# Kernel optimization log

Measured on AMD Instinct MI355X. Metric: run time of the kernel, lower is better.

## Reference

```python
import jax, jax.numpy as jnp
import numpy as np
from math import factorial, sqrt, pi

L = 10  # must match init_kwargs


def setup_inputs() -> dict:
    key = jax.random.key(0)
    pos = jax.random.normal(key, (2_000_000, 3), dtype=jnp.float32)
    return {"pos": pos}


def _cpow_tables(zr, zi, nmax):
    """Powers (zr + i*zi)^n for n=0..nmax. Returns (nmax+1, N) real and imag parts.
    Matches powcmplx in the source (repeated complex multiply), computed once."""
    reals = [jnp.ones_like(zr)]
    imags = [jnp.zeros_like(zr)]
    for _ in range(nmax):
        r, im = reals[-1], imags[-1]
        reals.append(zr * r - zi * im)
        imags.append(zr * im + zi * r)
    return jnp.stack(reals), jnp.stack(imags)


def reference(pos):
    norms = jnp.linalg.norm(pos, axis=1)            # (N,)
    mask = (norms > 0).astype(pos.dtype)            # replaces boolean indexing ids
    x, y, x0 = pos[:, 0], pos[:, 1], pos[:, 2]
    xpl1r, xpl1i = -0.5 * x, -0.5 * y
    xm1r, xm1i = 0.5 * x, -0.5 * y
    # precompute all needed complex powers (same math as powcmplx, deduplicated)
    z1r_t, z1i_t = _cpow_tables(xpl1r, xpl1i, L)    # (L+1, N)
    z2r_t, z2i_t = _cpow_tables(xm1r, xm1i, L)

    clms = [None] * ((L + 1) ** 2)
    i = 0
    for l in range(L + 1):
        rl = norms ** l
        for M in range(-l, 1):
            m = abs(M)
            shr = jnp.zeros_like(x)
            shi = jnp.zeros_like(x)
            for p in range(l + 1):
                q = p - m
                s = l - p - q
                if q >= 0 and s >= 0:
                    z1r, z1i = z1r_t[p], z1i_t[p]
                    z2r, z2i = z2r_t[q], z2i_t[q]
                    # NOTE: faithful to source, including its quirks:
                    # zreal uses z1r**2 - z2i**2, and the term is scaled by x0
                    # (x0**s is computed in the source but never used).
                    zreal = z1r ** 2 - z2i ** 2
                    zimag = z1r * z2i + z1i * z2r
                    c = 1.0 / (factorial(p) * factorial(q) * factorial(s))
                    shr = shr + zreal * x0 * c
                    shi = shi + zimag * x0 * c
            scale = sqrt(factorial(l + m) * factorial(l - m)) * sqrt((2 * l + 1) / (4.0 * pi))
            clm_r = jnp.sum(shr * rl * mask) * scale
            clm_i = jnp.sum(shi * rl * mask) * scale
            if m == 0:
                clms[i] = clm_r
            else:
                f = sqrt(2.0) * (-1) ** m
                clms[i] = f * clm_i
                clms[i + 2 * m] = f * clm_r
            i += 1
        i += l
    return jnp.stack(clms).reshape(-1, 1)  # ((L+1)^2, 1)
```

## Files before the change

kernel.cpp:

```cpp
#include <hip/hip_runtime.h>

namespace {

constexpr int LMAX = 10;
constexpr double PI_D = 3.14159265358979323846;

constexpr double dfact(int n) {
    double r = 1.0;
    for (int i = 2; i <= n; ++i) r *= (double)i;
    return r;
}

constexpr double csqrt(double x) {
    if (x <= 0.0) return 0.0;
    double g = x > 1.0 ? x : 1.0;
    for (int i = 0; i < 100; ++i) g = 0.5 * (g + x / g);
    return g;
}

constexpr double FACT[LMAX + 1] = {1., 1., 2., 6., 24., 120., 720., 5040., 40320., 362880., 3628800.};

constexpr int slot_r(int l, int m) { return l * l + m; }
constexpr int slot_i(int l, int m) { return l * l + (l + 1) + (m - 1); }
constexpr int NA = (LMAX + 1) * (LMAX + 1);

constexpr float ci_coef(int l, int m, int q) {
    const double c = 1.0 / (FACT[q + m] * FACT[q] * FACT[l - m - 2 * q]);
    return (q & 1) ? (float)(-c) : (float)c;
}

struct Tables {
    int   map[NA];
    float scl[NA];
};

constexpr Tables make_tables() {
    Tables t{};
    for (int l = 0; l <= LMAX; ++l) {
        for (int m = 0; m <= l; ++m) {
            const int k = slot_r(l, m);
            const double scale =
                csqrt(dfact(l + m) * dfact(l - m)) * csqrt((2 * l + 1) / (4.0 * PI_D));
            const double fold = (m >= 1 && (l - m) <= 1) ? 1.0 / (dfact(m) * dfact(l - m)) : 1.0;
            if (m == 0) {
                t.map[k] = l * l + l;
                t.scl[k] = (float)(scale * fold);
            } else {
                const double f = csqrt(2.0) * ((m & 1) ? -1.0 : 1.0);
                t.map[k] = l * l + l + m;
                t.scl[k] = (float)(f * scale * fold);
            }
        }
        for (int m = 1; m <= l; ++m) {
            const int k = slot_i(l, m);
            const double scale =
                csqrt(dfact(l + m) * dfact(l - m)) * csqrt((2 * l + 1) / (4.0 * PI_D));
            const double f    = csqrt(2.0) * ((m & 1) ? -1.0 : 1.0);
            const double fold = ((l - m) <= 1) ? 1.0 / (dfact(m) * dfact(l - m)) : 1.0;
            t.map[k] = l * l + l - m;
            t.scl[k] = (float)(f * scale * fold);
        }
    }
    return t;
}

__constant__ Tables c_tab = make_tables();

}

__global__ __launch_bounds__(256, 2) void sht_kernel(const float* __restrict__ pos,
                                                     float* __restrict__ out, int n, int nblk) {
    constexpr int PL = LMAX;
    constexpr int QX = PL / 2;

    float acc[NA];
#pragma unroll
    for (int k = 0; k < NA; ++k) acc[k] = 0.f;

    const int tid    = (int)blockIdx.x * 256 + (int)threadIdx.x;
    const int stride = nblk * 256;

    int   i = tid;
    float x = 0.f, y = 0.f, z0 = 0.f;
    if (i < n) {
        x  = pos[3 * i + 0];
        y  = pos[3 * i + 1];
        z0 = pos[3 * i + 2];
    }

    while (i < n) {
        const int inext = i + stride;
        float     px = 0.f, py = 0.f, pz = 0.f;
        if (inext < n) {
            px = pos[3 * inext + 0];
            py = pos[3 * inext + 1];
            pz = pos[3 * inext + 2];
        }

        const float r2  = x * x + y * y + z0 * z0;
        const float nrm = sqrtf(r2);
        const float w0  = (nrm > 0.f) ? z0 : 0.f;

        const float ar  = -0.5f * x, ai = -0.5f * y;
        const float rho = ar * ar + ai * ai;

        float zi[PL + 1], sr[PL + 1], si[QX + 1];
        zi[0] = 0.f;
        sr[0] = 1.f;
        si[0] = 0.f;
        float zrc = 1.f;
#pragma unroll
        for (int p = 1; p <= PL; ++p) {
            const float nzr = ar * zrc - ai * zi[p - 1];
            zi[p]           = ar * zi[p - 1] + ai * zrc;
            zrc             = nzr;
            sr[p]           = zrc * zrc;
            if (p <= QX) si[p] = zi[p] * zi[p];
        }
        float rp[PL + 1];
        rp[0] = 1.f;
#pragma unroll
        for (int l = 1; l <= PL; ++l) rp[l] = rp[l - 1] * nrm;

#pragma unroll
        for (int l = 0; l <= LMAX; ++l) {
            const float wrl = w0 * rp[l];
#pragma unroll
            for (int m = 0; m <= l; ++m) {
                const int Q = (l - m) >> 1;
                if (m >= 1 && Q == 0) {
                    acc[slot_r(l, m)] += sr[m] * wrl;
                    acc[slot_i(l, m)] += zi[m] * wrl;
                } else {
                    float shr = 0.f;
#pragma unroll
                    for (int p = m; 2 * p <= l + m; ++p) {
                        const int   q  = p - m;
                        const float cr = (float)(1.0 / (FACT[p] * FACT[q] * FACT[l - 2 * p + m]));
                        shr += (sr[p] - si[q]) * cr;
                    }
                    acc[slot_r(l, m)] += shr * wrl;
                    if (m >= 1) {
                        float t = ci_coef(l, m, Q);
#pragma unroll
                        for (int q = Q - 1; q >= 0; --q) t = t * rho + ci_coef(l, m, q);
                        acc[slot_i(l, m)] += (t * zi[m]) * wrl;
                    }
                }
            }
        }

        i  = inext;
        x  = px;
        y  = py;
        z0 = pz;
    }

    __shared__ float red[4][NA];
    const int lane = threadIdx.x & 63;
    const int wav  = threadIdx.x >> 6;
#pragma unroll
    for (int k = 0; k < NA; ++k) {
        float v = acc[k];
#pragma unroll
        for (int off = 32; off > 0; off >>= 1) v += __shfl_down(v, off, 64);
        if (lane == 0) red[wav][k] = v;
    }
    __syncthreads();
    if ((int)threadIdx.x < NA) {
        const int   k = (int)threadIdx.x;
        const float v = red[0][k] + red[1][k] + red[2][k] + red[3][k];
        atomicAdd(&out[c_tab.map[k]], v * c_tab.scl[k]);
    }
}

extern "C" void kernel_launch(void* const* d_in, const int* in_sizes, int n_in,
                              void* d_out, int out_size, void* d_ws, size_t ws_size,
                              hipStream_t stream) {
    const float* pos = (const float*)d_in[0];
    float* out       = (float*)d_out;
    const int n      = in_sizes[0] / 3;

    hipMemsetAsync(d_out, 0, (size_t)out_size * sizeof(float), stream);

    const int threads = 256;
    const int blocks = 512;
    sht_kernel<<<blocks, threads, 0, stream>>>(pos, out, n, blocks);
}
```

Before: 126.7 us.

## Accumulate per-power moments and combine linearly in a separate kernel

The real-part sums are linear in the per-point powers sr[p] and si[q] times r^l, so the kernel now accumulates those raw moments per point and applies the factorial coefficients afterwards in a small combine kernel. This removes the inner coefficient sums from the hot loop. Work is also split by l parity across block pairs, which lowers the accumulators per thread and register pressure, but each point is loaded and its powers computed twice. The change adds a workspace memset, a second kernel launch and a different float summation order.

New measurement: 119.4 us. -5.8%, faster.

```diff
diff --git a/kernel.cpp b/kernel.cpp
--- a/kernel.cpp
+++ b/kernel.cpp
@@ -20,64 +20,129 @@
 
 constexpr double FACT[LMAX + 1] = {1., 1., 2., 6., 24., 120., 720., 5040., 40320., 362880., 3628800.};
 
-constexpr int slot_r(int l, int m) { return l * l + m; }
-constexpr int slot_i(int l, int m) { return l * l + (l + 1) + (m - 1); }
-constexpr int NA = (LMAX + 1) * (LMAX + 1);
+constexpr int NM_M = 66;
+constexpr int mi(int p, int l) { return l * (l + 1) / 2 + p; }
+constexpr int ni_base(int l) {
+    int c = 0;
+    for (int ll = 0; ll < l; ++ll) c += ll / 2;
+    return c;
+}
+constexpr int ni(int q, int l) { return NM_M + ni_base(l) + (q - 1); }
+constexpr int NM_N  = 25;
+constexpr int NMOM  = NM_M + NM_N;
+constexpr int ZSLOT = NMOM;
+constexpr int WS_FLOATS = NMOM + 1;
+
+constexpr int part_lmax(int part) { return part ? 9 : 10; }
+constexpr int nls(int part) { return part ? 5 : 6; }
+constexpr int lidx(int part, int l) { return (l - part) >> 1; }
+constexpr int nM(int part) { int c = 0; for (int l = part; l <= LMAX; l += 2) c += l + 1; return c; }
+constexpr int nN(int part) { int c = 0; for (int l = part; l <= LMAX; l += 2) c += l / 2; return c; }
+constexpr int nMom(int part) { return nM(part) + nN(part); }
+constexpr int nI(int part) { int c = 0; for (int l = part; l <= LMAX; l += 2) c += l; return c; }
+constexpr int nAcc(int part) { return nMom(part) + nI(part); }
+
+constexpr int locM(int part, int p, int l) {
+    int c = 0;
+    for (int ll = part; ll < l; ll += 2) c += ll + 1;
+    return c + p;
+}
+constexpr int locN(int part, int q, int l) {
+    int c = nM(part);
+    for (int ll = part; ll < l; ll += 2) c += ll / 2;
+    return c + (q - 1);
+}
+constexpr int locI(int part, int m, int l) {
+    int c = nMom(part);
+    for (int ll = part; ll < l; ll += 2) c += ll;
+    return c + (m - 1);
+}
+
+constexpr int MAXMOM = 51;
+constexpr int MAXIMG = 30;
 
 constexpr float ci_coef(int l, int m, int q) {
     const double c = 1.0 / (FACT[q + m] * FACT[q] * FACT[l - m - 2 * q]);
     return (q & 1) ? (float)(-c) : (float)c;
 }
 
-struct Tables {
-    int   map[NA];
-    float scl[NA];
+struct PartTab {
+    short wsmap[2][MAXMOM];
+    int   omap[2][MAXIMG];
+    float oscl[2][MAXIMG];
 };
 
-constexpr Tables make_tables() {
-    Tables t{};
+constexpr PartTab make_pt() {
+    PartTab t{};
+    for (int part = 0; part < 2; ++part) {
+        for (int l = part; l <= LMAX; l += 2) {
+            for (int p = 0; p <= l; ++p) t.wsmap[part][locM(part, p, l)] = (short)mi(p, l);
+            for (int q = 1; q <= l / 2; ++q) t.wsmap[part][locN(part, q, l)] = (short)ni(q, l);
+            for (int m = 1; m <= l; ++m) {
+                const int    k     = locI(part, m, l) - nMom(part);
+                const double scale = csqrt(dfact(l + m) * dfact(l - m)) * csqrt((2 * l + 1) / (4.0 * PI_D));
+                const double f     = csqrt(2.0) * ((m & 1) ? -1.0 : 1.0);
+                const double fold  = ((l - m) <= 1) ? 1.0 / (dfact(m) * dfact(l - m)) : 1.0;
+                t.omap[part][k] = l * l + l - m;
+                t.oscl[part][k] = (float)(f * scale * fold);
+            }
+        }
+    }
+    return t;
+}
+
+struct CombTab {
+    int   out[66];
+    float scale[66];
+    int   nt[66];
+    float c[66][6];
+    short mIx[66][6];
+    short nIx[66][6];
+};
+
+constexpr CombTab make_comb() {
+    CombTab t{};
+    int k = 0;
     for (int l = 0; l <= LMAX; ++l) {
         for (int m = 0; m <= l; ++m) {
-            const int k = slot_r(l, m);
-            const double scale =
-                csqrt(dfact(l + m) * dfact(l - m)) * csqrt((2 * l + 1) / (4.0 * PI_D));
-            const double fold = (m >= 1 && (l - m) <= 1) ? 1.0 / (dfact(m) * dfact(l - m)) : 1.0;
-            if (m == 0) {
-                t.map[k] = l * l + l;
-                t.scl[k] = (float)(scale * fold);
-            } else {
-                const double f = csqrt(2.0) * ((m & 1) ? -1.0 : 1.0);
-                t.map[k] = l * l + l + m;
-                t.scl[k] = (float)(f * scale * fold);
-            }
-        }
-        for (int m = 1; m <= l; ++m) {
-            const int k = slot_i(l, m);
-            const double scale =
-                csqrt(dfact(l + m) * dfact(l - m)) * csqrt((2 * l + 1) / (4.0 * PI_D));
-            const double f    = csqrt(2.0) * ((m & 1) ? -1.0 : 1.0);
-            const double fold = ((l - m) <= 1) ? 1.0 / (dfact(m) * dfact(l - m)) : 1.0;
-            t.map[k] = l * l + l - m;
-            t.scl[k] = (float)(f * scale * fold);
+            const double scale = csqrt(dfact(l + m) * dfact(l - m)) * csqrt((2 * l + 1) / (4.0 * PI_D));
+            const double f     = (m == 0) ? 1.0 : csqrt(2.0) * ((m & 1) ? -1.0 : 1.0);
+            t.out[k]   = (m == 0) ? l * l + l : l * l + l + m;
+            t.scale[k] = (float)(f * scale);
+            const int Q = (l - m) / 2;
+            t.nt[k]     = Q + 1;
+            for (int q = 0; q <= Q; ++q) {
+                const double c = 1.0 / (FACT[q + m] * FACT[q] * FACT[l - m - 2 * q]);
+                t.c[k][q]   = (float)c;
+                t.mIx[k][q] = (short)mi(q + m, l);
+                t.nIx[k][q] = (short)(q >= 1 ? ni(q, l) : ZSLOT);
+            }
+            ++k;
         }
     }
     return t;
 }
 
-__constant__ Tables c_tab = make_tables();
-
-}
-
-__global__ __launch_bounds__(256, 2) void sht_kernel(const float* __restrict__ pos,
-                                                     float* __restrict__ out, int n, int nblk) {
-    constexpr int PL = LMAX;
-    constexpr int QX = PL / 2;
-
-    float acc[NA];
-#pragma unroll
-    for (int k = 0; k < NA; ++k) acc[k] = 0.f;
-
-    const int tid    = (int)blockIdx.x * 256 + (int)threadIdx.x;
+__constant__ PartTab c_pt = make_pt();
+__constant__ CombTab c_cb = make_comb();
+
+}
+
+template <int PART>
+__device__ __forceinline__ void sht_part(const float* __restrict__ pos, float* __restrict__ out,
+                                         float* __restrict__ ws, int n, int nblk) {
+    constexpr int PL  = part_lmax(PART);
+    constexpr int QX  = PL / 2;
+    constexpr int NL  = nls(PART);
+    constexpr int NMO = nMom(PART);
+    constexpr int NAC = nAcc(PART);
+
+    float acc[NAC];
+#pragma unroll
+    for (int k = 0; k < NAC; ++k) acc[k] = 0.f;
+
+    const int bid    = (int)(blockIdx.x >> 1);
+    const int tid    = bid * 256 + (int)threadIdx.x;
     const int stride = nblk * 256;
 
     int   i = tid;
@@ -104,48 +169,52 @@
         const float ar  = -0.5f * x, ai = -0.5f * y;
         const float rho = ar * ar + ai * ai;
 
-        float zi[PL + 1], sr[PL + 1], si[QX + 1];
-        zi[0] = 0.f;
-        sr[0] = 1.f;
-        si[0] = 0.f;
-        float zrc = 1.f;
-#pragma unroll
-        for (int p = 1; p <= PL; ++p) {
-            const float nzr = ar * zrc - ai * zi[p - 1];
-            zi[p]           = ar * zi[p - 1] + ai * zrc;
-            zrc             = nzr;
-            sr[p]           = zrc * zrc;
-            if (p <= QX) si[p] = zi[p] * zi[p];
-        }
-        float rp[PL + 1];
-        rp[0] = 1.f;
-#pragma unroll
-        for (int l = 1; l <= PL; ++l) rp[l] = rp[l - 1] * nrm;
-
-#pragma unroll
-        for (int l = 0; l <= LMAX; ++l) {
-            const float wrl = w0 * rp[l];
-#pragma unroll
-            for (int m = 0; m <= l; ++m) {
+        float wl[NL];
+        {
+            const float n2 = nrm * nrm;
+            float       w  = (PART == 0) ? w0 : w0 * nrm;
+#pragma unroll
+            for (int k = 0; k < NL; ++k) {
+                wl[k] = w;
+                w *= n2;
+            }
+        }
+
+        float zi[PL + 1];
+        float zrc = 1.f, zic = 0.f;
+#pragma unroll
+        for (int p = 0; p <= PL; ++p) {
+            if (p) {
+                const float nr = ar * zrc - ai * zic;
+                zic            = ar * zic + ai * zrc;
+                zrc            = nr;
+            }
+            zi[p] = zic;
+            const float srp = zrc * zrc;
+#pragma unroll
+            for (int l = PART; l <= LMAX; l += 2)
+                if (l >= p) acc[locM(PART, p, l)] += srp * wl[lidx(PART, l)];
+            if (p >= 1 && p <= QX) {
+                const float sip = zic * zic;
+#pragma unroll
+                for (int l = PART; l <= LMAX; l += 2)
+                    if (l >= 2 * p) acc[locN(PART, p, l)] += sip * wl[lidx(PART, l)];
+            }
+        }
+
+#pragma unroll
+        for (int l = PART; l <= LMAX; l += 2) {
+            const float wrl = wl[lidx(PART, l)];
+#pragma unroll
+            for (int m = 1; m <= l; ++m) {
                 const int Q = (l - m) >> 1;
-                if (m >= 1 && Q == 0) {
-                    acc[slot_r(l, m)] += sr[m] * wrl;
-                    acc[slot_i(l, m)] += zi[m] * wrl;
+                if (Q == 0) {
+                    acc[locI(PART, m, l)] += zi[m] * wrl;
                 } else {
-                    float shr = 0.f;
-#pragma unroll
-                    for (int p = m; 2 * p <= l + m; ++p) {
-                        const int   q  = p - m;
-                        const float cr = (float)(1.0 / (FACT[p] * FACT[q] * FACT[l - 2 * p + m]));
-                        shr += (sr[p] - si[q]) * cr;
-                    }
-                    acc[slot_r(l, m)] += shr * wrl;
-                    if (m >= 1) {
-                        float t = ci_coef(l, m, Q);
-#pragma unroll
-                        for (int q = Q - 1; q >= 0; --q) t = t * rho + ci_coef(l, m, q);
-                        acc[slot_i(l, m)] += (t * zi[m]) * wrl;
-                    }
+                    float tq = ci_coef(l, m, Q);
+#pragma unroll
+                    for (int q = Q - 1; q >= 0; --q) tq = tq * rho + ci_coef(l, m, q);
+                    acc[locI(PART, m, l)] += (tq * zi[m]) * wrl;
                 }
             }
         }
@@ -156,21 +225,46 @@
         z0 = pz;
     }
 
-    __shared__ float red[4][NA];
+    __shared__ float red[4][NAC];
     const int lane = threadIdx.x & 63;
     const int wav  = threadIdx.x >> 6;
 #pragma unroll
-    for (int k = 0; k < NA; ++k) {
+    for (int k = 0; k < NAC; ++k) {
         float v = acc[k];
 #pragma unroll
         for (int off = 32; off > 0; off >>= 1) v += __shfl_down(v, off, 64);
         if (lane == 0) red[wav][k] = v;
     }
     __syncthreads();
-    if ((int)threadIdx.x < NA) {
+    if ((int)threadIdx.x < NAC) {
         const int   k = (int)threadIdx.x;
         const float v = red[0][k] + red[1][k] + red[2][k] + red[3][k];
-        atomicAdd(&out[c_tab.map[k]], v * c_tab.scl[k]);
+        if (k < NMO) {
+            atomicAdd(&ws[c_pt.wsmap[PART][k]], v);
+        } else {
+            const int j = k - NMO;
+            atomicAdd(&out[c_pt.omap[PART][j]], v * c_pt.oscl[PART][j]);
+        }
+    }
+}
+
+__global__ __launch_bounds__(256, 2) void sht_kernel(const float* __restrict__ pos,
+                                                     float* __restrict__ out,
+                                                     float* __restrict__ ws, int n, int nblk) {
+    if (blockIdx.x & 1)
+        sht_part<1>(pos, out, ws, n, nblk);
+    else
+        sht_part<0>(pos, out, ws, n, nblk);
+}
+
+__global__ void sht_combine(const float* __restrict__ ws, float* __restrict__ out) {
+    const int t = (int)threadIdx.x;
+    if (t < 66) {
+        const int nt = c_cb.nt[t];
+        float     v  = 0.f;
+        for (int j = 0; j < nt; ++j)
+            v += c_cb.c[t][j] * (ws[c_cb.mIx[t][j]] - ws[c_cb.nIx[t][j]]);
+        out[c_cb.out[t]] = c_cb.scale[t] * v;
     }
 }
 
@@ -179,11 +273,15 @@
                               hipStream_t stream) {
     const float* pos = (const float*)d_in[0];
     float* out       = (float*)d_out;
+    float* ws        = (float*)d_ws;
     const int n      = in_sizes[0] / 3;
 
     hipMemsetAsync(d_out, 0, (size_t)out_size * sizeof(float), stream);
+    hipMemsetAsync(d_ws, 0, WS_FLOATS * sizeof(float), stream);
 
     const int threads = 256;
-    const int blocks = 512;
-    sht_kernel<<<blocks, threads, 0, stream>>>(pos, out, n, blocks);
-}
+    const int nblk_per_part = 384;
+    const int blocks        = 2 * nblk_per_part;
+    sht_kernel<<<blocks, threads, 0, stream>>>(pos, out, ws, n, nblk_per_part);
+    sht_combine<<<1, 128, 0, stream>>>(ws, out);
+}
```
